# Kernel tuning notes

Hardware: AMD Instinct MI355X
Metric: run time of the kernel (lower is better)

## Reference

```python
import jax, jax.numpy as jnp
import numpy as np

N = 100000
E = 1600000
EMB3 = 192   # embedding_size * 3
F_LAT = 64   # latency_feature_size
F_OUT = 128  # latency_feature_size * 2 (GATConv out_feats, 1 head)
NEG_SLOPE = 0.2  # DGL GATConv default leaky_relu slope


def setup_inputs() -> dict:
    key = jax.random.key(0)
    ks = jax.random.split(key, 9)
    return {
        "embed": jax.random.normal(ks[0], (N, EMB3), dtype=jnp.float32),
        "src": jax.random.randint(ks[1], (E,), 0, N, dtype=jnp.int64)
               if jax.config.jax_enable_x64 else jax.random.randint(ks[1], (E,), 0, N, dtype=jnp.int32),
        "dst": jax.random.randint(ks[2], (E,), 0, N, dtype=jnp.int32),
        "W_lin": jax.random.normal(ks[3], (EMB3, F_LAT), dtype=jnp.float32) * 0.05,
        "b_lin": jax.random.normal(ks[4], (F_LAT,), dtype=jnp.float32) * 0.05,
        "W_gat": jax.random.normal(ks[5], (F_LAT, F_OUT), dtype=jnp.float32) * 0.05,
        "attn_l": jax.random.normal(ks[6], (F_OUT,), dtype=jnp.float32) * 0.05,
        "attn_r": jax.random.normal(ks[7], (F_OUT,), dtype=jnp.float32) * 0.05,
        "b_gat": jax.random.normal(ks[8], (F_OUT,), dtype=jnp.float32) * 0.05,
    }


def reference(embed, src, dst, W_lin, b_lin, W_gat, attn_l, attn_r, b_gat):
    # linear_input + relu: [N, 192] -> [N, 64]
    x = jax.nn.relu(embed @ W_lin + b_lin)

    # GATConv (1 head): projection [N, 128]
    feat = x @ W_gat
    el = feat @ attn_l  # [N]
    er = feat @ attn_r  # [N]

    # per-edge attention logit with leaky relu
    e = jax.nn.leaky_relu(el[src] + er[dst], negative_slope=NEG_SLOPE)  # [E]

    # edge softmax over incoming edges of each dst node (segment softmax)
    emax = jax.ops.segment_max(e, dst, num_segments=N)           # [N], -inf for empty
    emax = jnp.where(jnp.isfinite(emax), emax, 0.0)
    ee = jnp.exp(e - emax[dst])                                   # [E]
    denom = jax.ops.segment_sum(ee, dst, num_segments=N)          # [N]
    denom = jnp.where(denom > 0, denom, 1.0)
    alpha = ee / denom[dst]                                       # [E]

    # weighted message aggregation: [N, 128]
    rst = jax.ops.segment_sum(feat[src] * alpha[:, None], dst, num_segments=N)
    y = rst + b_gat  # GATConv bias

    mu, logvar = jnp.split(y, 2, axis=-1)
    return mu, jnp.tanh(logvar)
```

## Files before the change

### kernel.cpp

```cpp
#include <hip/hip_runtime.h>
#include <hip/hip_bf16.h>

#define NEG_SLOPE 0.2f

typedef __attribute__((ext_vector_type(8))) short bf16x8;
typedef __attribute__((ext_vector_type(4))) float f32x4;

__device__ __forceinline__ unsigned pack_bf16(float a, float b) {
    unsigned ua = __float_as_uint(a), ub = __float_as_uint(b);
    ua += 0x7FFFu + ((ua >> 16) & 1u);
    ub += 0x7FFFu + ((ub >> 16) & 1u);
    return (ua >> 16) | (ub & 0xFFFF0000u);
}

__global__ __launch_bounds__(256) void k_gemm(
    const float* __restrict__ embed, const float* __restrict__ W_lin,
    const float* __restrict__ b_lin, const float* __restrict__ W_gat,
    const float* __restrict__ attn_l, const float* __restrict__ attn_r,
    unsigned* __restrict__ feat_u32, float* __restrict__ el,
    float* __restrict__ er, int N)
{
    __shared__ __align__(16) char lds[40960];
    const int t = threadIdx.x;
    const int lane = t & 63;
    const int w = t >> 6;
    const int lc = lane & 15;
    const int hg = lane >> 4;
    const int nb = blockIdx.x * 128;

    for (int i = t; i < 6144; i += 256) {
        const int c = i & 63, kp = i >> 6;
        const float w0 = W_lin[(2 * kp) * 64 + c];
        const float w1 = W_lin[(2 * kp + 1) * 64 + c];
        const unsigned off = (unsigned)(c * 384 + kp * 4) ^ ((c & 7) << 4);
        *(unsigned*)(lds + off) = pack_bf16(w0, w1);
    }
    for (int i = t; i < 4096; i += 256) {
        const int c = i & 127, kp = i >> 7;
        const float w0 = W_gat[(2 * kp) * 128 + c];
        const float w1 = W_gat[(2 * kp + 1) * 128 + c];
        const unsigned off = (unsigned)(c * 128 + kp * 4) ^ ((c & 7) << 4);
        *(unsigned*)(lds + 24576 + off) = pack_bf16(w0, w1);
    }
    __syncthreads();

    f32x4 acc1[2][4];
#pragma unroll
    for (int mt = 0; mt < 2; mt++)
#pragma unroll
        for (int nt = 0; nt < 4; nt++) acc1[mt][nt] = (f32x4)0.f;

#pragma unroll
    for (int ks = 0; ks < 6; ks++) {
        bf16x8 bfr[4];
#pragma unroll
        for (int nt = 0; nt < 4; nt++) {
            const int c = nt * 16 + lc;
            const unsigned off = (unsigned)(c * 384 + ks * 64 + hg * 16) ^ ((c & 7) << 4);
            bfr[nt] = *(const bf16x8*)(lds + off);
        }
#pragma unroll
        for (int mt = 0; mt < 2; mt++) {
            int row = nb + w * 32 + mt * 16 + lc;
            if (row >= N) row = N - 1;
            const float4* ep = (const float4*)(embed + (size_t)row * 192 + ks * 32 + hg * 8);
            const float4 p = ep[0], q = ep[1];
            union { bf16x8 v; unsigned u[4]; } a;
            a.u[0] = pack_bf16(p.x, p.y); a.u[1] = pack_bf16(p.z, p.w);
            a.u[2] = pack_bf16(q.x, q.y); a.u[3] = pack_bf16(q.z, q.w);
#pragma unroll
            for (int nt = 0; nt < 4; nt++)
                acc1[mt][nt] = __builtin_amdgcn_mfma_f32_16x16x32_bf16(a.v, bfr[nt], acc1[mt][nt], 0, 0, 0);
        }
    }

    float blv[4];
#pragma unroll
    for (int nt = 0; nt < 4; nt++) blv[nt] = b_lin[nt * 16 + lc];

    __syncthreads();

#pragma unroll
    for (int mt = 0; mt < 2; mt++)
#pragma unroll
        for (int nt = 0; nt < 4; nt++)
#pragma unroll
            for (int r = 0; r < 4; r++) {
                float v = acc1[mt][nt][r] + blv[nt];
                v = v > 0.f ? v : 0.f;
                const int xrow = w * 32 + mt * 16 + 4 * hg + r;
                const int col = nt * 16 + lc;
                const unsigned off = (unsigned)(xrow * 128 + col * 2) ^ ((xrow & 7) << 4);
                unsigned bv = __float_as_uint(v);
                bv += 0x7FFFu + ((bv >> 16) & 1u);
                *(unsigned short*)(lds + off) = (unsigned short)(bv >> 16);
            }
    __syncthreads();

    f32x4 acc2[2][8];
#pragma unroll
    for (int mt = 0; mt < 2; mt++)
#pragma unroll
        for (int nt = 0; nt < 8; nt++) acc2[mt][nt] = (f32x4)0.f;

#pragma unroll
    for (int ks = 0; ks < 2; ks++) {
        bf16x8 a2[2];
#pragma unroll
        for (int mt = 0; mt < 2; mt++) {
            const int row = w * 32 + mt * 16 + lc;
            const unsigned off = (unsigned)(row * 128 + ks * 64 + hg * 16) ^ ((row & 7) << 4);
            a2[mt] = *(const bf16x8*)(lds + off);
        }
#pragma unroll
        for (int nt = 0; nt < 8; nt++) {
            const int c = nt * 16 + lc;
            const unsigned off = (unsigned)(c * 128 + ks * 64 + hg * 16) ^ ((c & 7) << 4);
            const bf16x8 b2 = *(const bf16x8*)(lds + 24576 + off);
            acc2[0][nt] = __builtin_amdgcn_mfma_f32_16x16x32_bf16(a2[0], b2, acc2[0][nt], 0, 0, 0);
            acc2[1][nt] = __builtin_amdgcn_mfma_f32_16x16x32_bf16(a2[1], b2, acc2[1][nt], 0, 0, 0);
        }
    }

    float alv[8], arv[8];
#pragma unroll
    for (int nt = 0; nt < 8; nt++) {
        alv[nt] = attn_l[nt * 16 + lc];
        arv[nt] = attn_r[nt * 16 + lc];
    }

#pragma unroll
    for (int mt = 0; mt < 2; mt++) {
        const int rbase = nb + w * 32 + mt * 16 + 4 * hg;
#pragma unroll
        for (int nt = 0; nt < 4; nt++)
#pragma unroll
            for (int r = 0; r < 4; r++) {
                const int row = rbase + r;
                if (row < N)
                    feat_u32[(size_t)row * 64 + nt * 16 + lc] =
                        pack_bf16(acc2[mt][nt][r], acc2[mt][nt + 4][r]);
            }
        float elv[4] = {0.f, 0.f, 0.f, 0.f}, erv[4] = {0.f, 0.f, 0.f, 0.f};
#pragma unroll
        for (int nt = 0; nt < 8; nt++)
#pragma unroll
            for (int r = 0; r < 4; r++) {
                elv[r] = fmaf(acc2[mt][nt][r], alv[nt], elv[r]);
                erv[r] = fmaf(acc2[mt][nt][r], arv[nt], erv[r]);
            }
#pragma unroll
        for (int r = 0; r < 4; r++) {
#pragma unroll
            for (int o = 1; o < 16; o <<= 1) {
                elv[r] += __shfl_xor(elv[r], o, 64);
                erv[r] += __shfl_xor(erv[r], o, 64);
            }
            const int row = rbase + r;
            if (lc == r && row < N) { el[row] = elv[r]; er[row] = erv[r]; }
        }
    }
}

__global__ void k_hist(const int* __restrict__ dst, int* __restrict__ counts,
                       int* __restrict__ rank, int E) {
    const int i = (blockIdx.x * 256 + threadIdx.x) * 4;
    if (i + 3 < E) {
        const int4 v = *(const int4*)&dst[i];
        int4 r;
        r.x = atomicAdd(&counts[v.x], 1);
        r.y = atomicAdd(&counts[v.y], 1);
        r.z = atomicAdd(&counts[v.z], 1);
        r.w = atomicAdd(&counts[v.w], 1);
        *(int4*)&rank[i] = r;
    } else {
        for (int j = i; j < E; j++) rank[j] = atomicAdd(&counts[dst[j]], 1);
    }
}

__global__ __launch_bounds__(256) void k_scan1(
    const int* __restrict__ counts, int* __restrict__ offs,
    int* __restrict__ blocksums, int N)
{
    __shared__ int lds[256];
    const int t = threadIdx.x;
    const int base = blockIdx.x * 1024 + t * 4;
    int c0 = 0, c1 = 0, c2 = 0, c3 = 0;
    if (base + 3 < N) {
        int4 v = *(const int4*)&counts[base];
        c0 = v.x; c1 = v.y; c2 = v.z; c3 = v.w;
    } else {
        if (base + 0 < N) c0 = counts[base + 0];
        if (base + 1 < N) c1 = counts[base + 1];
        if (base + 2 < N) c2 = counts[base + 2];
        if (base + 3 < N) c3 = counts[base + 3];
    }
    const int s = c0 + c1 + c2 + c3;
    lds[t] = s;
    __syncthreads();
    for (int o = 1; o < 256; o <<= 1) {
        int u = (t >= o) ? lds[t - o] : 0;
        __syncthreads();
        lds[t] += u;
        __syncthreads();
    }
    const int excl = lds[t] - s;
    int o0 = excl, o1 = excl + c0, o2 = o1 + c1, o3 = o2 + c2;
    if (base + 3 < N) {
        *(int4*)&offs[base] = make_int4(o0, o1, o2, o3);
    } else {
        if (base + 0 < N) offs[base + 0] = o0;
        if (base + 1 < N) offs[base + 1] = o1;
        if (base + 2 < N) offs[base + 2] = o2;
        if (base + 3 < N) offs[base + 3] = o3;
    }
    if (t == 255) blocksums[blockIdx.x] = lds[255];
}

__global__ void k_scan2(int* __restrict__ blocksums, int nb) {
    __shared__ int lds[128];
    const int t = threadIdx.x;
    const int v = (t < nb) ? blocksums[t] : 0;
    lds[t] = v;
    __syncthreads();
    for (int o = 1; o < 128; o <<= 1) {
        int u = (t >= o) ? lds[t - o] : 0;
        __syncthreads();
        lds[t] += u;
        __syncthreads();
    }
    if (t < nb) blocksums[t] = lds[t] - v;
}

__global__ void k_scan3(int* __restrict__ offs, const int* __restrict__ blocksums,
                        int N, int E) {
    int i = blockIdx.x * 256 + threadIdx.x;
    if (i < N) offs[i] += blocksums[i >> 10];
    if (i == 0) offs[N] = E;
}

__global__ void k_scat(const int* __restrict__ src, const int* __restrict__ dst,
                       const int* __restrict__ rank, const int* __restrict__ offs,
                       int* __restrict__ csr, int E) {
    const int i = (blockIdx.x * 256 + threadIdx.x) * 4;
    if (i + 3 < E) {
        const int4 s4 = *(const int4*)&src[i];
        const int4 d4 = *(const int4*)&dst[i];
        const int4 r4 = *(const int4*)&rank[i];
        csr[offs[d4.x] + r4.x] = s4.x;
        csr[offs[d4.y] + r4.y] = s4.y;
        csr[offs[d4.z] + r4.z] = s4.z;
        csr[offs[d4.w] + r4.w] = s4.w;
    } else {
        for (int j = i; j < E; j++) csr[offs[dst[j]] + rank[j]] = src[j];
    }
}

__global__ __launch_bounds__(256) void k_agg(
    const int* __restrict__ csr, const int* __restrict__ offs,
    const float* __restrict__ el, const float* __restrict__ er,
    const unsigned* __restrict__ feat, const float* __restrict__ b_gat,
    float* __restrict__ out, int N)
{
    const int t = threadIdx.x;
    const int lane = t & 63;
    const int wid = t >> 6;
    const int d = blockIdx.x * 4 + wid;
    if (d >= N) return;
    const int start = offs[d];
    const int cnt = offs[d + 1] - start;
    const float erd = er[d];
    const int g = lane >> 3;
    const int i = lane & 7;

    float a0[8], a1[8];
#pragma unroll
    for (int k = 0; k < 8; k++) { a0[k] = 0.f; a1[k] = 0.f; }
    float sp = 0.f;

    for (int base = 0; base < cnt; base += 64) {
        const int idx = base + lane;
        const bool v = idx < cnt;
        const int sj = v ? csr[start + idx] : 0;
        float p = 0.f;
        if (v) {
            float e = el[sj] + erd;
            e = e >= 0.f ? e : NEG_SLOPE * e;
            p = __expf(e);
        }
        sp += p;

#pragma unroll
        for (int jj = 0; jj < 8; jj += 2) {
            if (base + jj * 8 >= cnt) break;
            const int s0 = __shfl(sj, jj * 8 + g, 64);
            const float p0 = __shfl(p, jj * 8 + g, 64);
            const int s1 = __shfl(sj, jj * 8 + 8 + g, 64);
            const float p1 = __shfl(p, jj * 8 + 8 + g, 64);
            const uint4* fp0 = (const uint4*)&feat[(size_t)s0 * 64 + i * 8];
            const uint4* fp1 = (const uint4*)&feat[(size_t)s1 * 64 + i * 8];
            const uint4 fa = fp0[0], fb = fp0[1];
            const uint4 fc = fp1[0], fd = fp1[1];
            const unsigned va[8] = {fa.x, fa.y, fa.z, fa.w, fb.x, fb.y, fb.z, fb.w};
            const unsigned vb[8] = {fc.x, fc.y, fc.z, fc.w, fd.x, fd.y, fd.z, fd.w};
#pragma unroll
            for (int k = 0; k < 8; k++) {
                a0[k] = fmaf(p0, __uint_as_float(va[k] << 16), a0[k]);
                a1[k] = fmaf(p0, __uint_as_float(va[k] & 0xFFFF0000u), a1[k]);
                a0[k] = fmaf(p1, __uint_as_float(vb[k] << 16), a0[k]);
                a1[k] = fmaf(p1, __uint_as_float(vb[k] & 0xFFFF0000u), a1[k]);
            }
        }
    }

#pragma unroll
    for (int k = 0; k < 8; k++) {
#pragma unroll
        for (int o = 8; o < 64; o <<= 1) {
            a0[k] += __shfl_xor(a0[k], o, 64);
            a1[k] += __shfl_xor(a1[k], o, 64);
        }
    }
#pragma unroll
    for (int o = 1; o < 64; o <<= 1) sp += __shfl_xor(sp, o, 64);

    const float inv = cnt ? 1.f / sp : 0.f;
    const size_t nh = (size_t)N * 64;

    if (g == 0) {
        float4 v0, v1;
        const float4 bg0 = *(const float4*)&b_gat[i * 8];
        const float4 bg1 = *(const float4*)&b_gat[i * 8 + 4];
        v0.x = a0[0] * inv + bg0.x; v0.y = a0[1] * inv + bg0.y;
        v0.z = a0[2] * inv + bg0.z; v0.w = a0[3] * inv + bg0.w;
        v1.x = a0[4] * inv + bg1.x; v1.y = a0[5] * inv + bg1.y;
        v1.z = a0[6] * inv + bg1.z; v1.w = a0[7] * inv + bg1.w;
        *(float4*)&out[(size_t)d * 64 + i * 8] = v0;
        *(float4*)&out[(size_t)d * 64 + i * 8 + 4] = v1;
    } else if (g == 1) {
        float4 v0, v1;
        const float4 bg0 = *(const float4*)&b_gat[64 + i * 8];
        const float4 bg1 = *(const float4*)&b_gat[64 + i * 8 + 4];
        v0.x = tanhf(a1[0] * inv + bg0.x); v0.y = tanhf(a1[1] * inv + bg0.y);
        v0.z = tanhf(a1[2] * inv + bg0.z); v0.w = tanhf(a1[3] * inv + bg0.w);
        v1.x = tanhf(a1[4] * inv + bg1.x); v1.y = tanhf(a1[5] * inv + bg1.y);
        v1.z = tanhf(a1[6] * inv + bg1.z); v1.w = tanhf(a1[7] * inv + bg1.w);
        *(float4*)&out[nh + (size_t)d * 64 + i * 8] = v0;
        *(float4*)&out[nh + (size_t)d * 64 + i * 8 + 4] = v1;
    }
}

extern "C" void kernel_launch(void* const* d_in, const int* in_sizes, int n_in,
                              void* d_out, int out_size, void* d_ws, size_t ws_size,
                              hipStream_t stream) {
    const float* embed  = (const float*)d_in[0];
    const int*   src    = (const int*)d_in[1];
    const int*   dst    = (const int*)d_in[2];
    const float* W_lin  = (const float*)d_in[3];
    const float* b_lin  = (const float*)d_in[4];
    const float* W_gat  = (const float*)d_in[5];
    const float* attn_l = (const float*)d_in[6];
    const float* attn_r = (const float*)d_in[7];
    const float* b_gat  = (const float*)d_in[8];
    float* out = (float*)d_out;

    const int N = in_sizes[0] / 192;
    const int E = in_sizes[1];

    char* ws = (char*)d_ws;
    size_t off = 0;
    auto alloc = [&](size_t bytes) -> void* {
        void* p = ws + off;
        off += (bytes + 255) & ~(size_t)255;
        return p;
    };
    unsigned* feat     = (unsigned*)alloc((size_t)N * 64 * 4);
    float*    el       = (float*)alloc((size_t)N * 4);
    float*    er       = (float*)alloc((size_t)N * 4);
    int*      counts   = (int*)alloc((size_t)N * 4);
    int*      offs     = (int*)alloc(((size_t)N + 1) * 4);
    int*      rank     = (int*)alloc((size_t)E * 4);
    int*      csr      = (int*)alloc((size_t)E * 4);
    int*      blocksums= (int*)alloc(1024 * 4);

    hipMemsetAsync(counts, 0, (size_t)N * 4, stream);

    k_gemm<<<(N + 127) / 128, 256, 0, stream>>>(embed, W_lin, b_lin, W_gat,
                                                attn_l, attn_r, feat, el, er, N);
    k_hist<<<(E / 4 + 255) / 256, 256, 0, stream>>>(dst, counts, rank, E);
    const int nb1 = (N + 1023) / 1024;
    k_scan1<<<nb1, 256, 0, stream>>>(counts, offs, blocksums, N);
    k_scan2<<<1, 128, 0, stream>>>(blocksums, nb1);
    k_scan3<<<(N + 255) / 256, 256, 0, stream>>>(offs, blocksums, N, E);
    k_scat<<<(E / 4 + 255) / 256, 256, 0, stream>>>(src, dst, rank, offs, csr, E);
    k_agg<<<(N + 3) / 4, 256, 0, stream>>>(csr, offs, el, er, feat, b_gat, out, N);
}
```

Measured before the change: 225.6 us.

## Aggregate messages with MFMA over 16-node destination tiles using fp16 features

Each wave now handles a tile of 16 consecutive destination nodes. It streams their CSR edges 32 at a time, gathers source feature rows into LDS, and builds a sparse one-hot-weighted A matrix so that an f16 MFMA does the weighted sum. A second MFMA against ones produces the softmax denominator. The features are stored as fp16 in natural column order instead of split bf16 halves, and CSR entries pack the local destination index into the upper bits of the source id. This trades scalar FMA work and per-node wave underutilisation for MFMA throughput, at the cost of packing assumptions (N < 2^20), fp16 range and precision, per-element LDS reads to build B, and uncoalesced scalar output stores.

```diff
diff --git a/kernel.cpp b/kernel.cpp
--- a/kernel.cpp
+++ b/kernel.cpp
@@ -1,5 +1,6 @@
 #include <hip/hip_runtime.h>
 #include <hip/hip_bf16.h>
+#include <hip/hip_fp16.h>
 
 #define NEG_SLOPE 0.2f
 
@@ -11,6 +12,12 @@
     ua += 0x7FFFu + ((ua >> 16) & 1u);
     ub += 0x7FFFu + ((ub >> 16) & 1u);
     return (ua >> 16) | (ub & 0xFFFF0000u);
+}
+
+__device__ __forceinline__ unsigned pack_f16(float a, float b) {
+    union { __half2 h; unsigned u; } cv;
+    cv.h = __floats2half2_rn(a, b);
+    return cv.u;
 }
 
 __global__ __launch_bounds__(256) void k_gemm(
@@ -133,13 +140,14 @@
     for (int mt = 0; mt < 2; mt++) {
         const int rbase = nb + w * 32 + mt * 16 + 4 * hg;
 #pragma unroll
-        for (int nt = 0; nt < 4; nt++)
+        for (int nt = 0; nt < 8; nt++)
 #pragma unroll
             for (int r = 0; r < 4; r++) {
+                const float V = acc2[mt][nt][r];
+                const float Vp = __shfl_xor(V, 1, 64);
                 const int row = rbase + r;
-                if (row < N)
-                    feat_u32[(size_t)row * 64 + nt * 16 + lc] =
-                        pack_bf16(acc2[mt][nt][r], acc2[mt][nt + 4][r]);
+                if (!(lc & 1) && row < N)
+                    feat_u32[(size_t)row * 64 + nt * 8 + (lc >> 1)] = pack_f16(V, Vp);
             }
         float elv[4] = {0.f, 0.f, 0.f, 0.f}, erv[4] = {0.f, 0.f, 0.f, 0.f};
 #pragma unroll
@@ -241,112 +249,120 @@
 
 __global__ void k_scat(const int* __restrict__ src, const int* __restrict__ dst,
                        const int* __restrict__ rank, const int* __restrict__ offs,
-                       int* __restrict__ csr, int E) {
+                       unsigned* __restrict__ csru, int E) {
     const int i = (blockIdx.x * 256 + threadIdx.x) * 4;
     if (i + 3 < E) {
         const int4 s4 = *(const int4*)&src[i];
         const int4 d4 = *(const int4*)&dst[i];
         const int4 r4 = *(const int4*)&rank[i];
-        csr[offs[d4.x] + r4.x] = s4.x;
-        csr[offs[d4.y] + r4.y] = s4.y;
-        csr[offs[d4.z] + r4.z] = s4.z;
-        csr[offs[d4.w] + r4.w] = s4.w;
+        csru[offs[d4.x] + r4.x] = (unsigned)s4.x | ((unsigned)(d4.x & 15) << 20);
+        csru[offs[d4.y] + r4.y] = (unsigned)s4.y | ((unsigned)(d4.y & 15) << 20);
+        csru[offs[d4.z] + r4.z] = (unsigned)s4.z | ((unsigned)(d4.z & 15) << 20);
+        csru[offs[d4.w] + r4.w] = (unsigned)s4.w | ((unsigned)(d4.w & 15) << 20);
     } else {
-        for (int j = i; j < E; j++) csr[offs[dst[j]] + rank[j]] = src[j];
+        for (int j = i; j < E; j++)
+            csru[offs[dst[j]] + rank[j]] = (unsigned)src[j] | ((unsigned)(dst[j] & 15) << 20);
     }
 }
 
 __global__ __launch_bounds__(256) void k_agg(
-    const int* __restrict__ csr, const int* __restrict__ offs,
+    const unsigned* __restrict__ csru, const int* __restrict__ offs,
     const float* __restrict__ el, const float* __restrict__ er,
     const unsigned* __restrict__ feat, const float* __restrict__ b_gat,
     float* __restrict__ out, int N)
 {
+    __shared__ __align__(16) char ldsB[32768];
     const int t = threadIdx.x;
     const int lane = t & 63;
     const int wid = t >> 6;
-    const int d = blockIdx.x * 4 + wid;
-    if (d >= N) return;
-    const int start = offs[d];
-    const int cnt = offs[d + 1] - start;
-    const float erd = er[d];
-    const int g = lane >> 3;
-    const int i = lane & 7;
-
-    float a0[8], a1[8];
-#pragma unroll
-    for (int k = 0; k < 8; k++) { a0[k] = 0.f; a1[k] = 0.f; }
-    float sp = 0.f;
-
-    for (int base = 0; base < cnt; base += 64) {
-        const int idx = base + lane;
-        const bool v = idx < cnt;
-        const int sj = v ? csr[start + idx] : 0;
+    const int lc = lane & 15;
+    const int hg = lane >> 4;
+    char* wlds = ldsB + wid * 8192;
+
+    const int ntiles = (N + 15) >> 4;
+    const int tile = blockIdx.x * 4 + wid;
+    if (tile >= ntiles) return;
+    const int d0 = tile << 4;
+    const int dmax = min(16, N - d0);
+
+    const int wstart = offs[d0];
+    const int wend = offs[d0 + dmax];
+
+    f32x4 accD[8];
+    f32x4 accDen = (f32x4)0.f;
+#pragma unroll
+    for (int nt = 0; nt < 8; nt++) accD[nt] = (f32x4)0.f;
+
+    union { bf16x8 v; unsigned u[4]; } ONESF;
+    ONESF.u[0] = ONESF.u[1] = ONESF.u[2] = ONESF.u[3] = 0x3C003C00u;
+
+    for (int w = wstart; w < wend; w += 32) {
+        const int eidx = w + lane;
+        const bool val = (lane < 32) && (eidx < wend);
+        const unsigned ev = val ? csru[eidx] : 0u;
+        const int sj = (int)(ev & 0xFFFFFu);
+        const int m = (int)((ev >> 20) & 15u);
         float p = 0.f;
-        if (v) {
-            float e = el[sj] + erd;
-            e = e >= 0.f ? e : NEG_SLOPE * e;
-            p = __expf(e);
-        }
-        sp += p;
-
-#pragma unroll
-        for (int jj = 0; jj < 8; jj += 2) {
-            if (base + jj * 8 >= cnt) break;
-            const int s0 = __shfl(sj, jj * 8 + g, 64);
-            const float p0 = __shfl(p, jj * 8 + g, 64);
-            const int s1 = __shfl(sj, jj * 8 + 8 + g, 64);
-            const float p1 = __shfl(p, jj * 8 + 8 + g, 64);
-            const uint4* fp0 = (const uint4*)&feat[(size_t)s0 * 64 + i * 8];
-            const uint4* fp1 = (const uint4*)&feat[(size_t)s1 * 64 + i * 8];
-            const uint4 fa = fp0[0], fb = fp0[1];
-            const uint4 fc = fp1[0], fd = fp1[1];
-            const unsigned va[8] = {fa.x, fa.y, fa.z, fa.w, fb.x, fb.y, fb.z, fb.w};
-            const unsigned vb[8] = {fc.x, fc.y, fc.z, fc.w, fd.x, fd.y, fd.z, fd.w};
-#pragma unroll
-            for (int k = 0; k < 8; k++) {
-                a0[k] = fmaf(p0, __uint_as_float(va[k] << 16), a0[k]);
-                a1[k] = fmaf(p0, __uint_as_float(va[k] & 0xFFFF0000u), a1[k]);
-                a0[k] = fmaf(p1, __uint_as_float(vb[k] << 16), a0[k]);
-                a1[k] = fmaf(p1, __uint_as_float(vb[k] & 0xFFFF0000u), a1[k]);
-            }
-        }
-    }
-
-#pragma unroll
-    for (int k = 0; k < 8; k++) {
-#pragma unroll
-        for (int o = 8; o < 64; o <<= 1) {
-            a0[k] += __shfl_xor(a0[k], o, 64);
-            a1[k] += __shfl_xor(a1[k], o, 64);
-        }
-    }
-#pragma unroll
-    for (int o = 1; o < 64; o <<= 1) sp += __shfl_xor(sp, o, 64);
-
-    const float inv = cnt ? 1.f / sp : 0.f;
+        if (val) {
+            float ee = el[sj] + er[d0 + m];
+            ee = ee >= 0.f ? ee : NEG_SLOPE * ee;
+            p = __expf(ee);
+        }
+
+#pragma unroll
+        for (int tt = 0; tt < 8; tt++) {
+            const int k = 4 * tt + hg;
+            const int rsrc = __shfl(sj, k, 64);
+            const uint4 gv = *(const uint4*)&feat[(size_t)rsrc * 64 + lc * 4];
+            const unsigned woff = ((unsigned)(k * 256 + lc * 16)) ^ (((unsigned)(tt >> 1) & 3u) << 4);
+            *(uint4*)(wlds + woff) = gv;
+        }
+
+        union { bf16x8 v; unsigned u[4]; } A;
+#pragma unroll
+        for (int jj = 0; jj < 4; jj++) {
+            const int sl = 8 * hg + 2 * jj;
+            const float p0 = __shfl(p, sl, 64);
+            const int   m0 = __shfl(m, sl, 64);
+            const float p1 = __shfl(p, sl + 1, 64);
+            const int   m1 = __shfl(m, sl + 1, 64);
+            A.u[jj] = pack_f16((m0 == lc) ? p0 : 0.f, (m1 == lc) ? p1 : 0.f);
+        }
+
+#pragma unroll
+        for (int nt = 0; nt < 8; nt++) {
+            union { bf16x8 v; unsigned short s[8]; } B;
+#pragma unroll
+            for (int j = 0; j < 8; j++) {
+                const unsigned roff = ((unsigned)((8 * hg + j) * 256 + (nt * 16 + lc) * 2))
+                                      ^ (((unsigned)hg & 3u) << 4);
+                B.s[j] = *(const unsigned short*)(wlds + roff);
+            }
+            accD[nt] = __builtin_amdgcn_mfma_f32_16x16x32_f16(A.v, B.v, accD[nt], 0, 0, 0);
+        }
+        accDen = __builtin_amdgcn_mfma_f32_16x16x32_f16(A.v, ONESF.v, accDen, 0, 0, 0);
+    }
+
+    float inv[4];
+#pragma unroll
+    for (int r = 0; r < 4; r++) {
+        const float den = accDen[r];
+        inv[r] = den > 0.f ? 1.f / den : 0.f;
+    }
+
     const size_t nh = (size_t)N * 64;
-
-    if (g == 0) {
-        float4 v0, v1;
-        const float4 bg0 = *(const float4*)&b_gat[i * 8];
-        const float4 bg1 = *(const float4*)&b_gat[i * 8 + 4];
-        v0.x = a0[0] * inv + bg0.x; v0.y = a0[1] * inv + bg0.y;
-        v0.z = a0[2] * inv + bg0.z; v0.w = a0[3] * inv + bg0.w;
-        v1.x = a0[4] * inv + bg1.x; v1.y = a0[5] * inv + bg1.y;
-        v1.z = a0[6] * inv + bg1.z; v1.w = a0[7] * inv + bg1.w;
-        *(float4*)&out[(size_t)d * 64 + i * 8] = v0;
-        *(float4*)&out[(size_t)d * 64 + i * 8 + 4] = v1;
-    } else if (g == 1) {
-        float4 v0, v1;
-        const float4 bg0 = *(const float4*)&b_gat[64 + i * 8];
-        const float4 bg1 = *(const float4*)&b_gat[64 + i * 8 + 4];
-        v0.x = tanhf(a1[0] * inv + bg0.x); v0.y = tanhf(a1[1] * inv + bg0.y);
-        v0.z = tanhf(a1[2] * inv + bg0.z); v0.w = tanhf(a1[3] * inv + bg0.w);
-        v1.x = tanhf(a1[4] * inv + bg1.x); v1.y = tanhf(a1[5] * inv + bg1.y);
-        v1.z = tanhf(a1[6] * inv + bg1.z); v1.w = tanhf(a1[7] * inv + bg1.w);
-        *(float4*)&out[nh + (size_t)d * 64 + i * 8] = v0;
-        *(float4*)&out[nh + (size_t)d * 64 + i * 8 + 4] = v1;
+#pragma unroll
+    for (int r = 0; r < 4; r++) {
+        const int d = d0 + 4 * hg + r;
+        if (d < N) {
+#pragma unroll
+            for (int nt = 0; nt < 8; nt++) {
+                const int c = nt * 16 + lc;
+                const float y = accD[nt][r] * inv[r] + b_gat[c];
+                if (c < 64) out[(size_t)d * 64 + c] = y;
+                else        out[nh + (size_t)d * 64 + (c - 64)] = tanhf(y);
+            }
+        }
     }
 }
 
@@ -380,7 +396,7 @@
     int*      counts   = (int*)alloc((size_t)N * 4);
     int*      offs     = (int*)alloc(((size_t)N + 1) * 4);
     int*      rank     = (int*)alloc((size_t)E * 4);
-    int*      csr      = (int*)alloc((size_t)E * 4);
+    unsigned* csru     = (unsigned*)alloc((size_t)E * 4);
     int*      blocksums= (int*)alloc(1024 * 4);
 
     hipMemsetAsync(counts, 0, (size_t)N * 4, stream);
@@ -392,6 +408,8 @@
     k_scan1<<<nb1, 256, 0, stream>>>(counts, offs, blocksums, N);
     k_scan2<<<1, 128, 0, stream>>>(blocksums, nb1);
     k_scan3<<<(N + 255) / 256, 256, 0, stream>>>(offs, blocksums, N, E);
-    k_scat<<<(E / 4 + 255) / 256, 256, 0, stream>>>(src, dst, rank, offs, csr, E);
-    k_agg<<<(N + 3) / 4, 256, 0, stream>>>(csr, offs, el, er, feat, b_gat, out, N);
-}
+    k_scat<<<(E / 4 + 255) / 256, 256, 0, stream>>>(src, dst, rank, offs, csru, E);
+
+    const int ntiles = (N + 15) / 16;
+    k_agg<<<(ntiles + 3) / 4, 256, 0, stream>>>(csru, offs, el, er, feat, b_gat, out, N);
+}
```

Result: slower. 238.1 us (+5.5%).
